# Performance work log

Measured on AMD Instinct MI355X. Metric: run time of the kernel, lower is better.

The kernel has to match this reference:

```python
import jax, jax.numpy as jnp
import numpy as np

FEAT_STRIDE = 16
PRE_NMS_TOP_N = 6000
POST_NMS_TOP_N = 300
NMS_THRESH = 0.7
A = 9  # len(scales)*len(ratios)
NEG = jnp.float32(-1e10)


def _generate_base_anchors(base_size=16, ratios=(0.5, 1.0, 2.0), scales=(8, 16, 32)):
    ratios = np.array(ratios, dtype=np.float64)
    scales = np.array(scales, dtype=np.float64)
    ctr = (base_size - 1) * 0.5
    size = float(base_size * base_size)
    ws = np.round(np.sqrt(size / ratios))
    hs = np.round(ws * ratios)
    out = []
    for w, h in zip(ws, hs):
        ws2 = w * scales
        hs2 = h * scales
        out.append(np.stack([ctr - 0.5 * (ws2 - 1), ctr - 0.5 * (hs2 - 1),
                             ctr + 0.5 * (ws2 - 1), ctr + 0.5 * (hs2 - 1)], axis=1))
    return np.concatenate(out, axis=0).astype(np.float32)  # [A,4]


def _all_anchors(H, W):
    base = _generate_base_anchors()
    sx = np.arange(W) * FEAT_STRIDE
    sy = np.arange(H) * FEAT_STRIDE
    sx, sy = np.meshgrid(sx, sy)  # [H,W] each, y-major ravel matches HW flatten
    shifts = np.stack([sx.ravel(), sy.ravel(), sx.ravel(), sy.ravel()], axis=1).astype(np.float32)
    return (shifts[:, None, :] + base[None, :, :]).reshape(-1, 4)  # [H*W*A,4]


def _nms_image(boxes, scores):
    # Greedy NMS on [N,4] boxes / [N] scores; emits top POST_NMS_TOP_N kept (padded with 0s).
    x1, y1, x2, y2 = boxes[:, 0], boxes[:, 1], boxes[:, 2], boxes[:, 3]
    areas = (x2 - x1 + 1.0) * (y2 - y1 + 1.0)

    def body(i, carry):
        live, ob, os_ = carry
        idx = jnp.argmax(live)
        s = live[idx]
        valid = s > NEG * 0.5
        b = boxes[idx]
        xx1 = jnp.maximum(b[0], x1)
        yy1 = jnp.maximum(b[1], y1)
        xx2 = jnp.minimum(b[2], x2)
        yy2 = jnp.minimum(b[3], y2)
        inter = jnp.maximum(xx2 - xx1 + 1.0, 0.0) * jnp.maximum(yy2 - yy1 + 1.0, 0.0)
        iou = inter / (areas[idx] + areas - inter)
        live = jnp.where(iou > NMS_THRESH, NEG, live)  # suppresses self too (iou=1)
        ob = ob.at[i].set(jnp.where(valid, b, 0.0))
        os_ = os_.at[i].set(jnp.where(valid, s, 0.0))
        return live, ob, os_

    init = (scores,
            jnp.zeros((POST_NMS_TOP_N, 4), boxes.dtype),
            jnp.zeros((POST_NMS_TOP_N,), scores.dtype))
    _, ob, os_ = jax.lax.fori_loop(0, POST_NMS_TOP_N, body, init)
    return ob, os_


def setup_inputs() -> dict:
    key = jax.random.key(0)
    ks = jax.random.split(key, 4)
    B, C, H, W = 4, 1024, 64, 64
    base_feat = jax.random.normal(ks[0], (B, C, H, W), jnp.float32)
    im_info = jnp.tile(jnp.array([H * 16.0, W * 16.0, 1.0], jnp.float32), (B, 1))
    gt_boxes = jnp.zeros((B, 20, 5), jnp.float32)   # unused in eval path
    num_boxes = jnp.zeros((B,), jnp.int32)           # unused in eval path
    conv_w = 0.01 * jax.random.normal(ks[1], (512, C, 3, 3), jnp.float32)
    conv_b = jnp.zeros((512,), jnp.float32)
    cls_w = 0.01 * jax.random.normal(ks[2], (2 * A, 512, 1, 1), jnp.float32)
    cls_b = jnp.zeros((2 * A,), jnp.float32)
    bbox_w = 0.01 * jax.random.normal(ks[3], (4 * A, 512, 1, 1), jnp.float32)
    bbox_b = jnp.zeros((4 * A,), jnp.float32)
    return {"base_feat": base_feat, "im_info": im_info, "gt_boxes": gt_boxes,
            "num_boxes": num_boxes, "conv_w": conv_w, "conv_b": conv_b,
            "cls_w": cls_w, "cls_b": cls_b, "bbox_w": bbox_w, "bbox_b": bbox_b}


def reference(base_feat, im_info, gt_boxes, num_boxes, conv_w, conv_b, cls_w, cls_b, bbox_w, bbox_b):
    B, _, H, W = base_feat.shape
    dn = ("NCHW", "OIHW", "NCHW")
    x = jax.lax.conv_general_dilated(base_feat, conv_w, (1, 1), [(1, 1), (1, 1)], dimension_numbers=dn)
    x = jax.nn.relu(x + conv_b[None, :, None, None])  # RPN_Conv + ReLU, [B,512,H,W]
    cls = jax.lax.conv_general_dilated(x, cls_w, (1, 1), "VALID", dimension_numbers=dn) + cls_b[None, :, None, None]
    bbox = jax.lax.conv_general_dilated(x, bbox_w, (1, 1), "VALID", dimension_numbers=dn) + bbox_b[None, :, None, None]

    # reshape(x,2) -> softmax over the 2-way axis: channel c pairs with c+A
    prob = jax.nn.softmax(cls.reshape(B, 2, A, H, W), axis=1)
    fg = prob[:, 1]                                   # [B,A,H,W] foreground probs
    scores = fg.transpose(0, 2, 3, 1).reshape(B, -1)  # [B, H*W*A]
    deltas = bbox.transpose(0, 2, 3, 1).reshape(B, -1, 4)

    anchors = jnp.asarray(_all_anchors(H, W))         # [H*W*A,4]
    wa = anchors[:, 2] - anchors[:, 0] + 1.0
    ha = anchors[:, 3] - anchors[:, 1] + 1.0
    cxa = anchors[:, 0] + 0.5 * (wa - 1.0)
    cya = anchors[:, 1] + 0.5 * (ha - 1.0)

    cx = deltas[..., 0] * wa + cxa
    cy = deltas[..., 1] * ha + cya
    pw = jnp.exp(deltas[..., 2]) * wa
    ph = jnp.exp(deltas[..., 3]) * ha
    x1 = cx - 0.5 * pw
    y1 = cy - 0.5 * ph
    x2 = cx + 0.5 * pw
    y2 = cy + 0.5 * ph

    imh = im_info[:, 0:1]
    imw = im_info[:, 1:2]
    x1 = jnp.clip(x1, 0.0, imw - 1.0)
    y1 = jnp.clip(y1, 0.0, imh - 1.0)
    x2 = jnp.clip(x2, 0.0, imw - 1.0)
    y2 = jnp.clip(y2, 0.0, imh - 1.0)
    boxes = jnp.stack([x1, y1, x2, y2], axis=-1)      # [B,N,4]

    s_top, idx = jax.lax.top_k(scores, PRE_NMS_TOP_N)
    b_top = jnp.take_along_axis(boxes, idx[:, :, None], axis=1)  # [B,6000,4]

    kept_boxes, kept_scores = jax.vmap(_nms_image)(b_top, s_top)  # [B,300,4],[B,300]
    bidx = jnp.broadcast_to(jnp.arange(B, dtype=kept_boxes.dtype).reshape(B, 1, 1),
                            (B, POST_NMS_TOP_N, 1))
    rois = jnp.concatenate([bidx, kept_boxes], axis=-1)  # [B,300,5]
    return rois, kept_scores
```

## Files before the change

### kernel.cpp

```cpp
#include <hip/hip_runtime.h>
#include <stdint.h>

#define HH_ 64
#define WW_ 64
#define NB 4
#define CIN 1024
#define CMID 512
#define NANCH (HH_*WW_*9)
#define PRE_N 6000
#define POST_N 300
#define CAND_PAD 6144
#define NEGV (-1.0e10f)
#define LO_SCL 2048.0f
#define LO_INV 4.8828125e-4f
#define MWORDS 192

typedef unsigned short u16;
typedef unsigned long long u64;
typedef __attribute__((ext_vector_type(8))) _Float16 f16x8;
typedef __attribute__((ext_vector_type(4))) float f32x4;

#define AS1 __attribute__((address_space(1)))
#define AS3 __attribute__((address_space(3)))

#define X_OFF   0
#define X_SZ    (NB*CMID*HH_*WW_)
#define SC_OFF  (X_OFF + X_SZ)
#define SC_SZ   (NB*NANCH)
#define BX_OFF  (SC_OFF + SC_SZ)
#define BX_SZ   (NB*NANCH*4)
#define CSC_OFF (BX_OFF + BX_SZ)
#define CSC_SZ  (NB*CAND_PAD)
#define CBX_OFF (CSC_OFF + CSC_SZ)
#define CBX_SZ  (NB*CAND_PAD*4)
#define CIX_OFF (CBX_OFF + CBX_SZ)
#define CIX_SZ  (NB*CAND_PAD)
#define WTH_OFF (CIX_OFF + CIX_SZ)
#define WTH_SZ  (9*512*1024/2)
#define WTL_OFF (WTH_OFF + WTH_SZ)
#define WTL_SZ  WTH_SZ
#define XH_OFF  (WTL_OFF + WTL_SZ)
#define XH_SZ   (NB*4096*1024/2)
#define XL_OFF  (XH_OFF + XH_SZ)
#define XL_SZ   XH_SZ
#define ZP_OFF  (XL_OFF + XL_SZ)
#define ZP_SZ   256

__device__ __forceinline__ void gl2lds16(const void* g, void* l) {
    __builtin_amdgcn_global_load_lds((const AS1 unsigned int*)g,
                                     (AS3 unsigned int*)l, 16, 0, 0);
}
union fh_u { _Float16 h; u16 u; };
__device__ __forceinline__ u16 f2h_hi(float x) {
    fh_u c; c.h = (_Float16)x; return c.u;
}
__device__ __forceinline__ u16 f2h_lo(float x, u16 hi) {
    fh_u c; c.u = hi;
    float hf = (float)c.h;
    fh_u d; d.h = (_Float16)((x - hf) * LO_SCL);
    return d.u;
}
__device__ __forceinline__ int cperm(int c) {
    int blk = c >> 5, w = c & 31;
    int pos = (w < 16) ? (((w >> 2) << 3) + (w & 3))
                       : ((((w - 16) >> 2) << 3) + 4 + (w & 3));
    return (blk << 5) + pos;
}
__device__ __forceinline__ unsigned fflip(unsigned u) {
    return (u & 0x80000000u) ? ~u : (u | 0x80000000u);
}

#define WT_BLKS 18432
__global__ __launch_bounds__(256) void prep_all(
    const float* __restrict__ conv_w, u16* __restrict__ WTH,
    u16* __restrict__ WTL, float* __restrict__ ZP,
    const float* __restrict__ in, u16* __restrict__ XH,
    u16* __restrict__ XL)
{
    __shared__ float T[64][65];
    const int tid = threadIdx.x;
    if (blockIdx.x < WT_BLKS) {
        int o = blockIdx.x * 256 + tid;
        int ci = o & 1023, co = (o >> 10) & 511, r = o >> 19;
        float v = conv_w[((size_t)(co * 1024 + ci)) * 9 + r];
        u16 h  = f2h_hi(v);
        u16 lo = f2h_lo(v, h);
        size_t d = (((size_t)(r * 512 + co)) << 10) + cperm(ci);
        WTH[d] = h; WTL[d] = lo;
        if (o < 256) ZP[o] = 0.f;
    } else {
        const int blk = blockIdx.x - WT_BLKS;
        const int b   = blk >> 10;
        const int ci0 = ((blk >> 6) & 15) << 6;
        const int sp0 = (blk & 63) << 6;
        const int tq  = tid >> 6;
        const int t64 = tid & 63;
#pragma unroll
        for (int w = 0; w < 16; w++) {
            int ci_l = w * 4 + tq;
            T[ci_l][t64] = in[(((size_t)(b * 1024 + ci0 + ci_l)) << 12) + sp0 + t64];
        }
        __syncthreads();
#pragma unroll
        for (int w = 0; w < 16; w++) {
            int sp_l = w * 4 + tq;
            float x = T[t64][sp_l];
            u16 h  = f2h_hi(x);
            u16 lo = f2h_lo(x, h);
            size_t d = (((size_t)((b << 12) + sp0 + sp_l)) << 10) + ci0 + cperm(t64);
            XH[d] = h; XL[d] = lo;
        }
    }
}

__global__ __launch_bounds__(256, 2) void conv3_mfma(
    const u16* __restrict__ WTH, const u16* __restrict__ WTL,
    const u16* __restrict__ XH, const u16* __restrict__ XL,
    const u16* __restrict__ ZP, const float* __restrict__ bias,
    float* __restrict__ Xout)
{
    __shared__ u16 Ah_s[2][4096];
    __shared__ u16 Al_s[2][4096];
    __shared__ u16 Bh_s[2][4096];
    __shared__ u16 Bl_s[2][4096];

    const int tid = threadIdx.x;
    const int bn  = blockIdx.x;
    const int bm  = blockIdx.y;
    const int l   = tid & 63;
    const int wid = tid >> 6, wm = wid >> 1, wn = wid & 1;

    const int rowq = tid >> 2;
    const int c8   = (((tid & 3) ^ ((tid >> 3) & 3)) << 3);

    int spb[2]; unsigned vmq[2];
#pragma unroll
    for (int q = 0; q < 2; q++) {
        int n = bn * 128 + q * 64 + rowq;
        int yy = (n >> 6) & 63, xx = n & 63;
        spb[q] = n;
        unsigned m9 = 0;
#pragma unroll
        for (int rr = 0; rr < 9; rr++) {
            int dy = rr / 3 - 1, dx = rr % 3 - 1;
            if ((unsigned)(yy + dy) < 64u && (unsigned)(xx + dx) < 64u)
                m9 |= 1u << rr;
        }
        vmq[q] = m9;
    }

    f32x4 acc0[4][4], acc1[4][4];
#pragma unroll
    for (int i = 0; i < 4; i++)
#pragma unroll
        for (int j = 0; j < 4; j++) { acc0[i][j] = (f32x4)0.f; acc1[i][j] = (f32x4)0.f; }

    const int NK = 288;

    auto stage = [&](int sb, int kt) {
        const int r   = kt >> 5;
        const int ci0 = (kt & 31) << 5;
        const int kr  = (r * 11) >> 5;
        const int sh  = (kr - 1) * 64 + (r - 3 * kr - 1);
        const size_t wbase = (((size_t)(r * 512 + bm * 128)) << 10) + ci0 + c8;
        u16* ah = &Ah_s[sb][tid * 8];
        u16* al = &Al_s[sb][tid * 8];
        u16* bh = &Bh_s[sb][tid * 8];
        u16* bl = &Bl_s[sb][tid * 8];
#pragma unroll
        for (int q = 0; q < 2; q++) {
            const size_t aoff = wbase + (((size_t)(q * 64 + rowq)) << 10);
            gl2lds16(WTH + aoff, ah + q * 2048);
            gl2lds16(WTL + aoff, al + q * 2048);
            const bool v = (vmq[q] >> r) & 1u;
            const size_t boff = (((size_t)(spb[q] + sh)) << 10) + ci0 + c8;
            gl2lds16(v ? (XH + boff) : ZP, bh + q * 2048);
            gl2lds16(v ? (XL + boff) : ZP, bl + q * 2048);
        }
    };

    const int lo16 = l & 15, hi4 = l >> 4;
    const int swl  = (lo16 >> 1) & 3;
    const int pch  = (hi4 ^ swl) << 3;
    const int aoff = (wm * 64 + lo16) * 32 + pch;
    const int boff = (wn * 64 + lo16) * 32 + pch;

    stage(0, 0);
    int buf = 0;
    for (int kt = 0; kt < NK; ++kt) {
        __syncthreads();
        f16x8 ah[4], av[4], bh[4], bv[4];
#pragma unroll
        for (int i = 0; i < 4; i++) {
            ah[i] = *(const f16x8*)&Ah_s[buf][aoff + i * 512];
            av[i] = *(const f16x8*)&Al_s[buf][aoff + i * 512];
            bh[i] = *(const f16x8*)&Bh_s[buf][boff + i * 512];
            bv[i] = *(const f16x8*)&Bl_s[buf][boff + i * 512];
        }
        if (kt + 1 < NK) stage(buf ^ 1, kt + 1);
#pragma unroll
        for (int mi = 0; mi < 4; mi++)
#pragma unroll
            for (int ni = 0; ni < 4; ni++) {
                acc0[mi][ni] = __builtin_amdgcn_mfma_f32_16x16x32_f16(
                    ah[mi], bh[ni], acc0[mi][ni], 0, 0, 0);
                acc1[mi][ni] = __builtin_amdgcn_mfma_f32_16x16x32_f16(
                    ah[mi], bv[ni], acc1[mi][ni], 0, 0, 0);
                acc1[mi][ni] = __builtin_amdgcn_mfma_f32_16x16x32_f16(
                    av[mi], bh[ni], acc1[mi][ni], 0, 0, 0);
            }
        buf ^= 1;
    }

#pragma unroll
    for (int mi = 0; mi < 4; mi++) {
        const int co0 = bm * 128 + wm * 64 + mi * 16 + ((l >> 4) << 2);
        const f32x4 b4 = *(const f32x4*)&bias[co0];
#pragma unroll
        for (int ni = 0; ni < 4; ni++) {
            const int n = bn * 128 + wn * 64 + ni * 16 + (l & 15);
            const int b = n >> 12, sp = n & 4095;
            f32x4 v0 = acc0[mi][ni], v1 = acc1[mi][ni];
            float* xo = Xout + (((size_t)(b * 512 + co0)) << 12) + sp;
            xo[0]        = fmaxf(fmaf(v1[0], LO_INV, v0[0]) + b4[0], 0.f);
            xo[4096]     = fmaxf(fmaf(v1[1], LO_INV, v0[1]) + b4[1], 0.f);
            xo[2 * 4096] = fmaxf(fmaf(v1[2], LO_INV, v0[2]) + b4[2], 0.f);
            xo[3 * 4096] = fmaxf(fmaf(v1[3], LO_INV, v0[3]) + b4[3], 0.f);
        }
    }
}

__global__ __launch_bounds__(128) void heads_kernel(
    const float* __restrict__ X, const float* __restrict__ cls_w,
    const float* __restrict__ cls_b, const float* __restrict__ bbox_w,
    const float* __restrict__ bbox_b, const float* __restrict__ im_info,
    float* __restrict__ SC, float* __restrict__ BXo)
{
    __shared__ __attribute__((aligned(16))) float Ws[54][256];
    const int tid = threadIdx.x;
    const int blk = blockIdx.x;
    const int b   = blk >> 5;
    const int s   = ((blk & 31) << 7) + tid;

    float acc[54];
#pragma unroll
    for (int j = 0; j < 18; j++) acc[j] = cls_b[j];
#pragma unroll
    for (int j = 0; j < 36; j++) acc[18 + j] = bbox_b[j];

    const float* xp = X + (size_t)b * CMID * 4096 + s;
    for (int c0 = 0; c0 < 512; c0 += 256) {
        __syncthreads();
        for (int e = tid; e < 54 * 256; e += 128) {
            int j = e >> 8, ci = e & 255;
            Ws[j][ci] = (j < 18) ? cls_w[j * 512 + c0 + ci]
                                 : bbox_w[(j - 18) * 512 + c0 + ci];
        }
        __syncthreads();
        for (int ci = 0; ci < 256; ci += 4) {
            float x0 = xp[(size_t)(c0 + ci) * 4096];
            float x1 = xp[(size_t)(c0 + ci + 1) * 4096];
            float x2 = xp[(size_t)(c0 + ci + 2) * 4096];
            float x3 = xp[(size_t)(c0 + ci + 3) * 4096];
#pragma unroll
            for (int j = 0; j < 54; j++) {
                float4 w4 = *(const float4*)&Ws[j][ci];
                acc[j] = fmaf(x3, w4.w, fmaf(x2, w4.z, fmaf(x1, w4.y, fmaf(x0, w4.x, acc[j]))));
            }
        }
    }

    const float imh = im_info[b * 3 + 0];
    const float imw = im_info[b * 3 + 1];
    const int hh = s >> 6, ww = s & 63;
    const float cxa = 7.5f + 16.f * (float)ww;
    const float cya = 7.5f + 16.f * (float)hh;
    const float WA[9] = {184.f, 368.f, 736.f, 128.f, 256.f, 512.f, 88.f, 176.f, 352.f};
    const float HA[9] = {96.f, 192.f, 384.f, 128.f, 256.f, 512.f, 176.f, 352.f, 704.f};
    const size_t base = (size_t)b * NANCH + (size_t)s * 9;
#pragma unroll
    for (int c = 0; c < 9; c++) {
        float bg = acc[c], fg = acc[9 + c];
        float m  = fmaxf(bg, fg);
        float e0 = expf(bg - m), e1 = expf(fg - m);
        float p  = e1 / (e0 + e1);
        float dx = acc[18 + 4 * c], dy = acc[19 + 4 * c];
        float dw = acc[20 + 4 * c], dh = acc[21 + 4 * c];
        float wa = WA[c], ha = HA[c];
        float cx = dx * wa + cxa;
        float cy = dy * ha + cya;
        float pw = expf(dw) * wa;
        float ph = expf(dh) * ha;
        float x1 = cx - 0.5f * pw, y1 = cy - 0.5f * ph;
        float x2 = cx + 0.5f * pw, y2 = cy + 0.5f * ph;
        x1 = fminf(fmaxf(x1, 0.f), imw - 1.f);
        y1 = fminf(fmaxf(y1, 0.f), imh - 1.f);
        x2 = fminf(fmaxf(x2, 0.f), imw - 1.f);
        y2 = fminf(fmaxf(y2, 0.f), imh - 1.f);
        SC[base + c] = p;
        *(float4*)&BXo[(base + c) * 4] = make_float4(x1, y1, x2, y2);
    }
}

__global__ __launch_bounds__(1024) void selsort_kernel(
    const float* __restrict__ SC, const float* __restrict__ BX,
    float* __restrict__ CSC, float* __restrict__ CBX, int* __restrict__ CIX)
{
    const int b = blockIdx.x, tid = threadIdx.x;
    const int lane = tid & 63, wv = tid >> 6;
    const float* sc = SC + (size_t)b * NANCH;
    const unsigned* bits = (const unsigned*)sc;

    __shared__ u64 sk[8704];
    unsigned* s_buf = (unsigned*)sk;
    __shared__ unsigned s_part[1024];
    __shared__ unsigned s_wsum[16];
    __shared__ unsigned s_sel[2];
    __shared__ int s_cnt;
    auto P = [](int i) { return i + (i >> 4); };

    auto findbin = [&](int nb, int bpt, unsigned target) -> uint2 {
        unsigned mysum = 0;
        const int base = tid * bpt;
        if (base < nb)
            for (int q = 0; q < bpt; q++) mysum += s_buf[base + q];
        s_part[tid] = mysum;
        unsigned wsum = mysum;
#pragma unroll
        for (int off = 32; off; off >>= 1) wsum += __shfl_down(wsum, off);
        if (lane == 0) s_wsum[wv] = wsum;
        __syncthreads();
        unsigned cum = 0;
        for (int w = wv + 1; w < 16; w++) cum += s_wsum[w];
        for (int ll = lane + 1; ll < 64; ll++) cum += s_part[(wv << 6) + ll];
        if (base < nb) {
            unsigned c = cum;
            for (int q = bpt - 1; q >= 0; q--) {
                unsigned h = s_buf[base + q];
                if (c < target && c + h >= target) { s_sel[0] = base + q; s_sel[1] = c; }
                c += h;
            }
        }
        __syncthreads();
        uint2 r; r.x = s_sel[0]; r.y = s_sel[1];
        __syncthreads();
        return r;
    };

    for (int i = tid; i < 8192; i += 1024) s_buf[i] = 0;
    __syncthreads();
    for (int i = tid; i < NANCH; i += 1024)
        atomicAdd(&s_buf[bits[i] >> 19], 1u);
    __syncthreads();
    uint2 r1 = findbin(8192, 8, PRE_N);
    const unsigned B1 = r1.x;
    unsigned target2 = PRE_N - r1.y;

    for (int i = tid; i < 8192; i += 1024) s_buf[i] = 0;
    __syncthreads();
    for (int i = tid; i < NANCH; i += 1024) {
        unsigned u = bits[i];
        if ((u >> 19) == B1) atomicAdd(&s_buf[(u >> 6) & 8191u], 1u);
    }
    __syncthreads();
    uint2 r2 = findbin(8192, 8, target2);
    const unsigned B2 = r2.x;
    unsigned target3 = target2 - r2.y;

    if (tid < 64) s_buf[tid] = 0;
    __syncthreads();
    const unsigned pref26 = (B1 << 13) | B2;
    for (int i = tid; i < NANCH; i += 1024) {
        unsigned u = bits[i];
        if ((u >> 6) == pref26) atomicAdd(&s_buf[u & 63u], 1u);
    }
    __syncthreads();
    uint2 r3 = findbin(64, 1, target3);
    const unsigned ustar = (B1 << 19) | (B2 << 6) | r3.x;

    for (int i = tid; i < 8704; i += 1024) sk[i] = 0ull;
    if (tid == 0) s_cnt = 0;
    __syncthreads();
    for (int i = tid; i < NANCH; i += 1024) {
        unsigned u = bits[i];
        if (u >= ustar) {
            int p = atomicAdd(&s_cnt, 1);
            if (p < 8192)
                sk[P(p)] = ((u64)fflip(u) << 32) | (u64)(~((unsigned)i));
        }
    }
    __syncthreads();

    for (int k = 2; k <= 8192; k <<= 1) {
        for (int j = k >> 1; j > 0; j >>= 1) {
            for (int t = tid; t < 8192; t += 1024) {
                int ixj = t ^ j;
                if (ixj > t) {
                    int pa = P(t), pb = P(ixj);
                    u64 a = sk[pa], c2 = sk[pb];
                    bool up = ((t & k) == 0);
                    if ((a < c2) == up) { sk[pa] = c2; sk[pb] = a; }
                }
            }
            __syncthreads();
        }
    }

    float* csc = CSC + (size_t)b * CAND_PAD;
    int*   cix = CIX + (size_t)b * CAND_PAD;
    float4* cbx4 = (float4*)CBX + (size_t)b * CAND_PAD;
    const float4* bx4 = (const float4*)BX + (size_t)b * NANCH;
    for (int i = tid; i < CAND_PAD; i += 1024) {
        if (i < PRE_N) {
            u64 key = sk[P(i)];
            unsigned khi = (unsigned)(key >> 32), klo = (unsigned)key;
            unsigned su = (khi & 0x80000000u) ? (khi ^ 0x80000000u) : ~khi;
            float scv = __uint_as_float(su);
            int ci = (int)(~klo);
            csc[i] = scv; cix[i] = ci;
            float4 pb;
            if (scv > -5.0e9f && (unsigned)ci < (unsigned)NANCH) pb = bx4[ci];
            else pb = make_float4(-4e9f, -4e9f, -4e9f, -4e9f);
            cbx4[i] = pb;
        } else {
            csc[i] = -2.0e10f;
            cix[i] = 0x7fffffff;
            cbx4[i] = make_float4(-4e9f, -4e9f, -4e9f, -4e9f);
        }
    }
}

__global__ __launch_bounds__(256) void nms_mask(
    const float* __restrict__ CBX, unsigned* __restrict__ MASK)
{
    const int rg = blockIdx.x, b = blockIdx.y, tid = threadIdx.x;
    const float4* cbx = (const float4*)CBX + (size_t)b * CAND_PAD;
    unsigned* mrow = MASK + (size_t)b * CAND_PAD * MWORDS;

    __shared__ float4 rb[64];
    __shared__ float  rar[64];
    __shared__ float4 cb[1024];
    __shared__ float  car[1024];

    if (tid < 64) {
        float4 v = cbx[rg * 64 + tid];
        rb[tid] = v;
        rar[tid] = (v.z - v.x + 1.f) * (v.w - v.y + 1.f);
    }
    __syncthreads();
    const int rl = tid >> 2;
    const int wq = tid & 3;
    const float4 rv = rb[rl];
    const float  ra = rar[rl];
    const size_t rbase = (size_t)(rg * 64 + rl) * MWORDS;

    for (int jt = rg >> 4; jt < 6; jt++) {
        __syncthreads();
        for (int e = tid; e < 1024; e += 256) {
            float4 v = cbx[jt * 1024 + e];
            cb[e] = v;
            car[e] = (v.z - v.x + 1.f) * (v.w - v.y + 1.f);
        }
        __syncthreads();
#pragma unroll
        for (int k = 0; k < 8; k++) {
            const int wt = wq + 4 * k;
            unsigned bits = 0;
            for (int bit = 0; bit < 32; bit++) {
                const int j = wt * 32 + bit;
                float4 cv = cb[j];
                float xx1 = fmaxf(rv.x, cv.x);
                float yy1 = fmaxf(rv.y, cv.y);
                float xx2 = fminf(rv.z, cv.z);
                float yy2 = fminf(rv.w, cv.w);
                float iw = fmaxf(xx2 - xx1 + 1.f, 0.f);
                float ih = fmaxf(yy2 - yy1 + 1.f, 0.f);
                float inter = iw * ih;
                float iou = inter / (ra + car[j] - inter);
                if (iou > 0.7f) bits |= (1u << bit);
            }
            mrow[rbase + jt * 32 + wt] = bits;
        }
    }
}

__global__ __launch_bounds__(64) void nms_scan(
    const float* __restrict__ CSC, const float* __restrict__ CBX,
    const unsigned* __restrict__ MASK, float* __restrict__ out)
{
    const int b = blockIdx.x, lane = threadIdx.x;
    const float*  csc = CSC + (size_t)b * CAND_PAD;
    const float4* cbx = (const float4*)CBX + (size_t)b * CAND_PAD;
    const unsigned* mk = MASK + (size_t)b * CAND_PAD * MWORDS;

    float* rois = out + (size_t)b * 1500;
    float* oscr = out + 6000 + (size_t)b * 300;

    for (int it = lane; it < POST_N; it += 64) {
        float* r = rois + it * 5;
        r[0] = (float)b; r[1] = 0.f; r[2] = 0.f; r[3] = 0.f; r[4] = 0.f;
        oscr[it] = 0.f;
    }
    __syncthreads();

    unsigned rm0 = 0u, rm1 = 0u, rm2 = 0u;
    int cnt = 0;
    unsigned rlo = mk[(size_t)lane * MWORDS + 0];
    unsigned rhi = mk[(size_t)lane * MWORDS + 1];
    float    rsc = csc[lane];

    for (int c = 0; c < 94 && cnt < POST_N; c++) {
        const int W0 = 2 * c;
        const int slot = W0 >> 6;
        unsigned sel = (slot == 0) ? rm0 : (slot == 1) ? rm1 : rm2;
        unsigned gw = __shfl(sel, (W0 & 63) + (lane >> 5));
        bool alive = !((gw >> (lane & 31)) & 1u) && (rsc > -5.0e9f);
        u64 rem = __ballot(alive);
        u64 keptm = 0ull;
        while (rem) {
            int sl = __builtin_ctzll(rem);
            keptm |= 1ull << sl;
            unsigned blo = __shfl(rlo, sl);
            unsigned bhi = __shfl(rhi, sl);
            rem &= ~(((u64)bhi << 32) | (u64)blo);
            rem &= ~(1ull << sl);
        }
        if (c + 1 < 94) {
            const int i2 = (c + 1) * 64 + lane;
            rlo = mk[(size_t)i2 * MWORDS + 2 * (c + 1)];
            rhi = mk[(size_t)i2 * MWORDS + 2 * (c + 1) + 1];
            rsc = csc[i2];
        }
        while (keptm && cnt < POST_N) {
            int sl = __builtin_ctzll(keptm);
            keptm &= keptm - 1ull;
            const int i = c * 64 + sl;
            const size_t rb = (size_t)i * MWORDS;
            rm0 |= mk[rb + lane];
            rm1 |= mk[rb + lane + 64];
            rm2 |= mk[rb + lane + 128];
            if (lane == 0) {
                float4 pb = cbx[i];
                float* r = rois + cnt * 5;
                r[1] = pb.x; r[2] = pb.y; r[3] = pb.z; r[4] = pb.w;
                oscr[cnt] = csc[i];
            }
            cnt++;
        }
    }
}

extern "C" void kernel_launch(void* const* d_in, const int* in_sizes, int n_in,
                              void* d_out, int out_size, void* d_ws, size_t ws_size,
                              hipStream_t stream)
{
    const float* base_feat = (const float*)d_in[0];
    const float* im_info   = (const float*)d_in[1];
    const float* conv_w    = (const float*)d_in[4];
    const float* conv_b    = (const float*)d_in[5];
    const float* cls_w     = (const float*)d_in[6];
    const float* cls_b     = (const float*)d_in[7];
    const float* bbox_w    = (const float*)d_in[8];
    const float* bbox_b    = (const float*)d_in[9];

    float* ws  = (float*)d_ws;
    float* X   = ws + X_OFF;
    float* SC  = ws + SC_OFF;
    float* BX  = ws + BX_OFF;
    float* CSC = ws + CSC_OFF;
    float* CBX = ws + CBX_OFF;
    int*   CIX = (int*)(ws + CIX_OFF);
    u16*   WTH = (u16*)(ws + WTH_OFF);
    u16*   WTL = (u16*)(ws + WTL_OFF);
    u16*   XHp = (u16*)(ws + XH_OFF);
    u16*   XLp = (u16*)(ws + XL_OFF);
    float* ZPf = ws + ZP_OFF;
    const u16* ZPu = (const u16*)ZPf;
    unsigned* MASK = (unsigned*)(ws + X_OFF);
    float* out = (float*)d_out;

    hipLaunchKernelGGL(prep_all, dim3(WT_BLKS + 4096), dim3(256), 0, stream,
                       conv_w, WTH, WTL, ZPf, base_feat, XHp, XLp);
    hipLaunchKernelGGL(conv3_mfma, dim3(128, 4), dim3(256), 0, stream,
                       WTH, WTL, XHp, XLp, ZPu, conv_b, X);
    hipLaunchKernelGGL(heads_kernel, dim3(128), dim3(128), 0, stream,
                       X, cls_w, cls_b, bbox_w, bbox_b, im_info, SC, BX);
    hipLaunchKernelGGL(selsort_kernel, dim3(4), dim3(1024), 0, stream,
                       SC, BX, CSC, CBX, CIX);
    hipLaunchKernelGGL(nms_mask, dim3(96, 4), dim3(256), 0, stream,
                       CBX, MASK);
    hipLaunchKernelGGL(nms_scan, dim3(4), dim3(64), 0, stream,
                       CSC, CBX, MASK, out);
}
```

Baseline: 1.222 ms.

## Split prep kernel, raise MFMA wave priority, drop LDS staging in heads kernel

The fused prep kernel is split into separate weight and activation conversion kernels. The MFMA inner loop in the conv kernel is wrapped in s_setprio so those waves are favoured while they issue matrix instructions. The heads kernel stops staging the 1x1 weights in shared memory and reads them directly from global memory through the cache, and it moves to 256-thread blocks with half as many blocks. The heads change halves the block count to 64 on a GPU with many compute units and puts weight loads on the global path, so that stage may lose parallelism.

```diff
diff --git a/kernel.cpp b/kernel.cpp
--- a/kernel.cpp
+++ b/kernel.cpp
@@ -70,46 +70,45 @@
     return (u & 0x80000000u) ? ~u : (u | 0x80000000u);
 }
 
-#define WT_BLKS 18432
-__global__ __launch_bounds__(256) void prep_all(
+__global__ __launch_bounds__(256) void prep_wtk(
     const float* __restrict__ conv_w, u16* __restrict__ WTH,
-    u16* __restrict__ WTL, float* __restrict__ ZP,
-    const float* __restrict__ in, u16* __restrict__ XH,
-    u16* __restrict__ XL)
+    u16* __restrict__ WTL, float* __restrict__ ZP)
+{
+    int o = blockIdx.x * 256 + threadIdx.x;
+    int ci = o & 1023, co = (o >> 10) & 511, r = o >> 19;
+    float v = conv_w[((size_t)(co * 1024 + ci)) * 9 + r];
+    u16 h  = f2h_hi(v);
+    u16 lo = f2h_lo(v, h);
+    size_t d = (((size_t)(r * 512 + co)) << 10) + cperm(ci);
+    WTH[d] = h; WTL[d] = lo;
+    if (o < 256) ZP[o] = 0.f;
+}
+
+__global__ __launch_bounds__(256) void prep_act(
+    const float* __restrict__ in, u16* __restrict__ XH, u16* __restrict__ XL)
 {
     __shared__ float T[64][65];
+    const int blk = blockIdx.x;
+    const int b   = blk >> 10;
+    const int ci0 = ((blk >> 6) & 15) << 6;
+    const int sp0 = (blk & 63) << 6;
     const int tid = threadIdx.x;
-    if (blockIdx.x < WT_BLKS) {
-        int o = blockIdx.x * 256 + tid;
-        int ci = o & 1023, co = (o >> 10) & 511, r = o >> 19;
-        float v = conv_w[((size_t)(co * 1024 + ci)) * 9 + r];
-        u16 h  = f2h_hi(v);
-        u16 lo = f2h_lo(v, h);
-        size_t d = (((size_t)(r * 512 + co)) << 10) + cperm(ci);
-        WTH[d] = h; WTL[d] = lo;
-        if (o < 256) ZP[o] = 0.f;
-    } else {
-        const int blk = blockIdx.x - WT_BLKS;
-        const int b   = blk >> 10;
-        const int ci0 = ((blk >> 6) & 15) << 6;
-        const int sp0 = (blk & 63) << 6;
-        const int tq  = tid >> 6;
-        const int t64 = tid & 63;
-#pragma unroll
-        for (int w = 0; w < 16; w++) {
-            int ci_l = w * 4 + tq;
-            T[ci_l][t64] = in[(((size_t)(b * 1024 + ci0 + ci_l)) << 12) + sp0 + t64];
-        }
-        __syncthreads();
-#pragma unroll
-        for (int w = 0; w < 16; w++) {
-            int sp_l = w * 4 + tq;
-            float x = T[t64][sp_l];
-            u16 h  = f2h_hi(x);
-            u16 lo = f2h_lo(x, h);
-            size_t d = (((size_t)((b << 12) + sp0 + sp_l)) << 10) + ci0 + cperm(t64);
-            XH[d] = h; XL[d] = lo;
-        }
+    const int tq  = tid >> 6;
+    const int t64 = tid & 63;
+#pragma unroll
+    for (int w = 0; w < 16; w++) {
+        int ci_l = w * 4 + tq;
+        T[ci_l][t64] = in[(((size_t)(b * 1024 + ci0 + ci_l)) << 12) + sp0 + t64];
+    }
+    __syncthreads();
+#pragma unroll
+    for (int w = 0; w < 16; w++) {
+        int sp_l = w * 4 + tq;
+        float x = T[t64][sp_l];
+        u16 h  = f2h_hi(x);
+        u16 lo = f2h_lo(x, h);
+        size_t d = (((size_t)((b << 12) + sp0 + sp_l)) << 10) + ci0 + cperm(t64);
+        XH[d] = h; XL[d] = lo;
     }
 }
 
@@ -198,6 +197,7 @@
             bv[i] = *(const f16x8*)&Bl_s[buf][boff + i * 512];
         }
         if (kt + 1 < NK) stage(buf ^ 1, kt + 1);
+        __builtin_amdgcn_s_setprio(1);
 #pragma unroll
         for (int mi = 0; mi < 4; mi++)
 #pragma unroll
@@ -209,6 +209,7 @@
                 acc1[mi][ni] = __builtin_amdgcn_mfma_f32_16x16x32_f16(
                     av[mi], bh[ni], acc1[mi][ni], 0, 0, 0);
             }
+        __builtin_amdgcn_s_setprio(0);
         buf ^= 1;
     }
 
@@ -230,17 +231,16 @@
     }
 }
 
-__global__ __launch_bounds__(128) void heads_kernel(
+__global__ __launch_bounds__(256) void heads_kernel(
     const float* __restrict__ X, const float* __restrict__ cls_w,
     const float* __restrict__ cls_b, const float* __restrict__ bbox_w,
     const float* __restrict__ bbox_b, const float* __restrict__ im_info,
     float* __restrict__ SC, float* __restrict__ BXo)
 {
-    __shared__ __attribute__((aligned(16))) float Ws[54][256];
     const int tid = threadIdx.x;
     const int blk = blockIdx.x;
-    const int b   = blk >> 5;
-    const int s   = ((blk & 31) << 7) + tid;
+    const int b   = blk >> 4;
+    const int s   = ((blk & 15) << 8) + tid;
 
     float acc[54];
 #pragma unroll
@@ -249,24 +249,17 @@
     for (int j = 0; j < 36; j++) acc[18 + j] = bbox_b[j];
 
     const float* xp = X + (size_t)b * CMID * 4096 + s;
-    for (int c0 = 0; c0 < 512; c0 += 256) {
-        __syncthreads();
-        for (int e = tid; e < 54 * 256; e += 128) {
-            int j = e >> 8, ci = e & 255;
-            Ws[j][ci] = (j < 18) ? cls_w[j * 512 + c0 + ci]
-                                 : bbox_w[(j - 18) * 512 + c0 + ci];
-        }
-        __syncthreads();
-        for (int ci = 0; ci < 256; ci += 4) {
-            float x0 = xp[(size_t)(c0 + ci) * 4096];
-            float x1 = xp[(size_t)(c0 + ci + 1) * 4096];
-            float x2 = xp[(size_t)(c0 + ci + 2) * 4096];
-            float x3 = xp[(size_t)(c0 + ci + 3) * 4096];
-#pragma unroll
-            for (int j = 0; j < 54; j++) {
-                float4 w4 = *(const float4*)&Ws[j][ci];
-                acc[j] = fmaf(x3, w4.w, fmaf(x2, w4.z, fmaf(x1, w4.y, fmaf(x0, w4.x, acc[j]))));
-            }
+    for (int ci = 0; ci < 512; ci += 4) {
+        float x0 = xp[(size_t)(ci) * 4096];
+        float x1 = xp[(size_t)(ci + 1) * 4096];
+        float x2 = xp[(size_t)(ci + 2) * 4096];
+        float x3 = xp[(size_t)(ci + 3) * 4096];
+#pragma unroll
+        for (int j = 0; j < 54; j++) {
+            const float* wp = (j < 18) ? (cls_w + j * 512 + ci)
+                                       : (bbox_w + (j - 18) * 512 + ci);
+            float4 w4 = *(const float4*)wp;
+            acc[j] = fmaf(x3, w4.w, fmaf(x2, w4.z, fmaf(x1, w4.y, fmaf(x0, w4.x, acc[j]))));
         }
     }
 
@@ -579,11 +572,13 @@
     unsigned* MASK = (unsigned*)(ws + X_OFF);
     float* out = (float*)d_out;
 
-    hipLaunchKernelGGL(prep_all, dim3(WT_BLKS + 4096), dim3(256), 0, stream,
-                       conv_w, WTH, WTL, ZPf, base_feat, XHp, XLp);
+    hipLaunchKernelGGL(prep_wtk, dim3(18432), dim3(256), 0, stream,
+                       conv_w, WTH, WTL, ZPf);
+    hipLaunchKernelGGL(prep_act, dim3(4096), dim3(256), 0, stream,
+                       base_feat, XHp, XLp);
     hipLaunchKernelGGL(conv3_mfma, dim3(128, 4), dim3(256), 0, stream,
                        WTH, WTL, XHp, XLp, ZPu, conv_b, X);
-    hipLaunchKernelGGL(heads_kernel, dim3(128), dim3(128), 0, stream,
+    hipLaunchKernelGGL(heads_kernel, dim3(64), dim3(256), 0, stream,
                        X, cls_w, cls_b, bbox_w, bbox_b, im_info, SC, BX);
     hipLaunchKernelGGL(selsort_kernel, dim3(4), dim3(1024), 0, stream,
                        SC, BX, CSC, CBX, CIX);
```

Result: slower. 1.386 ms (+13.4%).
